# Kernel optimization log

Hardware: AMD Instinct MI355X
Metric: run time of the kernel (lower is better)

## Reference

```python
import jax, jax.numpy as jnp
import numpy as np

N, D, IN, HID, OUT, E = 20000, 8, 64, 128, 64, 100000
EPS = 1e-5


def _bn(h, g, b):
    # training-mode BatchNorm1d: biased batch variance, eps=1e-5
    m = h.mean(axis=0)
    v = jnp.mean((h - m) ** 2, axis=0)
    return (h - m) * jax.lax.rsqrt(v + EPS) * g + b


def setup_inputs() -> dict:
    key = jax.random.key(0)
    ks = jax.random.split(key, 12)
    x = jax.random.normal(ks[0], (N, IN), dtype=jnp.float32)
    node_ts = jax.random.uniform(ks[1], (N,), dtype=jnp.float32)
    neighbor_idx = jax.random.randint(ks[2], (N, D), 0, N, dtype=jnp.int32)
    neighbor_ts = jax.random.uniform(ks[3], (N, D), dtype=jnp.float32)
    target = jax.random.randint(ks[4], (2, E), 0, N, dtype=jnp.int32)
    neg_pairs = jax.random.randint(ks[5], (2, E), 0, N, dtype=jnp.int32)
    W1 = jax.random.normal(ks[6], (IN, HID), dtype=jnp.float32) * (1.0 / np.sqrt(IN))
    b1 = jnp.zeros((HID,), jnp.float32)
    g1 = jnp.ones((HID,), jnp.float32)
    be1 = jnp.zeros((HID,), jnp.float32)
    W2 = jax.random.normal(ks[7], (HID, OUT), dtype=jnp.float32) * (1.0 / np.sqrt(HID))
    b2 = jnp.zeros((OUT,), jnp.float32)
    g2 = jnp.ones((OUT,), jnp.float32)
    be2 = jnp.zeros((OUT,), jnp.float32)
    Wd = jax.random.normal(ks[8], (OUT, 1), dtype=jnp.float32) * (1.0 / np.sqrt(OUT))
    bd = jnp.zeros((1,), jnp.float32)
    return {"x": x, "node_ts": node_ts, "neighbor_idx": neighbor_idx,
            "neighbor_ts": neighbor_ts, "target": target, "neg_pairs": neg_pairs,
            "W1": W1, "b1": b1, "g1": g1, "be1": be1,
            "W2": W2, "b2": b2, "g2": g2, "be2": be2, "Wd": Wd, "bd": bd}


def reference(x, node_ts, neighbor_idx, neighbor_ts, target, neg_pairs,
              W1, b1, g1, be1, W2, b2, g2, be2, Wd, bd):
    n = jnp.arange(N, dtype=neighbor_idx.dtype)
    # ---- level-2 queries: every node at its own timestamp ----
    # children = D temporal-neighbor slots + self (self always valid, ts=node_ts)
    c_idx = jnp.concatenate([neighbor_idx, n[:, None]], axis=1)          # [N, D+1]
    c_ts = jnp.concatenate([neighbor_ts, node_ts[:, None]], axis=1)      # [N, D+1]
    mask2 = jnp.concatenate([neighbor_ts <= node_ts[:, None],
                             jnp.ones((N, 1), bool)], axis=1)            # [N, D+1]
    # ---- level-1 queries: each (child node, child ts) pair ----
    ci = c_idx.reshape(-1)                                               # [M]
    cts = c_ts.reshape(-1)
    gc_idx = jnp.concatenate([neighbor_idx[ci], ci[:, None]], axis=1)    # [M, D+1]
    mask1 = jnp.concatenate([neighbor_ts[ci] <= cts[:, None],
                             jnp.ones((ci.shape[0], 1), bool)], axis=1)
    # ---- layer 0: raw features of grandchildren ----
    h0 = x[gc_idx]                                                       # [M, D+1, IN]
    m1 = mask1.astype(x.dtype)
    agg1 = jnp.einsum('mk,mkf->mf', m1, h0) / m1.sum(1, keepdims=True)   # masked mean
    h1 = jax.nn.relu(_bn(agg1 @ W1 + b1, g1, be1))                       # [M, HID]
    h1 = h1.reshape(N, D + 1, HID)
    # ---- layer 2 aggregation over temporal children ----
    m2 = mask2.astype(x.dtype)
    agg2 = jnp.einsum('nk,nkf->nf', m2, h1) / m2.sum(1, keepdims=True)
    embs = jax.nn.relu(_bn(agg2 @ W2 + b2, g2, be2))                     # [N, OUT]
    # ---- HadNet link decoder + BCEWithLogits ----
    pos = (embs[target[0]] * embs[target[1]]) @ Wd + bd                  # [E, 1]
    neg = (embs[neg_pairs[0]] * embs[neg_pairs[1]]) @ Wd + bd            # [E, 1]
    preds = jnp.concatenate([pos, neg], axis=0)[:, 0]                    # [2E]
    labels = jnp.concatenate([jnp.ones((E,), x.dtype), jnp.zeros((E,), x.dtype)])
    loss = jnp.mean(jnp.maximum(preds, 0.0) - preds * labels
                    + jnp.log1p(jnp.exp(-jnp.abs(preds))))
    return loss
```

## Files before the change

### kernel.cpp

```cpp
#include <hip/hip_runtime.h>
#include <math.h>

constexpr int kN = 20000;
constexpr int kD = 8;
constexpr int kE = 100000;
constexpr int kM = kN * 9;
constexpr int kTiles1 = kM / 16;
constexpr int kTiles3 = kN / 16;
constexpr float kEps = 1e-5f;

constexpr int S_SUM1 = 0, S_SQ1 = 128, S_SUM2 = 256, S_SQ2 = 320;

constexpr size_t REG_B     = 23040000;
constexpr size_t OFF_AGG2  = 46080000;
constexpr size_t OFF_STATS = 51200000;
constexpr size_t OFF_PRE2  = 0;
constexpr size_t OFF_EMBS  = 5120000;
constexpr size_t OFF_EMBSW = 10240000;

typedef short short8 __attribute__((ext_vector_type(8)));
typedef float floatx4 __attribute__((ext_vector_type(4)));

__device__ __forceinline__ unsigned f2bf(float f) {
  unsigned u = __float_as_uint(f);
  u += 0x7fffu + ((u >> 16) & 1u);
  return u >> 16;
}

__global__ __launch_bounds__(256) void k1a_gather(
    const float* __restrict__ x, const float* __restrict__ node_ts,
    const int* __restrict__ nidx, const float* __restrict__ nts,
    unsigned short* __restrict__ agg1)
{
  const int m = blockIdx.x * 4 + (threadIdx.x >> 6);
  const int lane = threadIdx.x & 63;
  const int n = (int)((unsigned)m / 9u);
  const int slot = m - n * 9;
  int c; float t;
  if (slot < kD) { c = nidx[n * kD + slot]; t = nts[n * kD + slot]; }
  else           { c = n;                   t = node_ts[n]; }
  c = __builtin_amdgcn_readfirstlane(c);
  float s = x[c * 64 + lane];
  float fcnt = 1.f;
#pragma unroll
  for (int j = 0; j < kD; ++j) {
    int cj = nidx[c * kD + j];
    float w = (nts[c * kD + j] <= t) ? 1.f : 0.f;
    s = fmaf(w, x[cj * 64 + lane], s);
    fcnt += w;
  }
  float v = s / fcnt;
  const int tt = m >> 4, r = m & 15, g = lane >> 3, jj = lane & 7;
  agg1[tt * 1024 + g * 128 + r * 8 + jj] = (unsigned short)f2bf(v);
}

__global__ __launch_bounds__(256, 3) void k1b_gemm1(
    const unsigned short* aggA,
    unsigned short* preLo,
    unsigned short* __restrict__ preHi,
    const float* __restrict__ W1, const float* __restrict__ b1,
    float* __restrict__ stats)
{
  __shared__ unsigned short W1T[128 * 72];
  __shared__ float redS[256][8];
  __shared__ float redQ[256][8];

  const int tid = threadIdx.x;
  const int lane = tid & 63;
  const int wave = tid >> 6;
  const int l15 = lane & 15;
  const int q = lane >> 4;

  for (int i = tid; i < 8192; i += 256) {
    int n = i >> 6, k = i & 63;
    W1T[n * 72 + k] = (unsigned short)f2bf(W1[k * 128 + n]);
  }
  __syncthreads();

  short8 bf[8][2];
#pragma unroll
  for (int c = 0; c < 8; ++c)
#pragma unroll
    for (int s = 0; s < 2; ++s)
      bf[c][s] = *(const short8*)&W1T[(c * 16 + l15) * 72 + q * 8 + s * 32];

  float b1c[8];
#pragma unroll
  for (int c = 0; c < 8; ++c) b1c[c] = b1[c * 16 + l15];

  float sum8[8], sq8[8];
#pragma unroll
  for (int c = 0; c < 8; ++c) { sum8[c] = 0.f; sq8[c] = 0.f; }

  const int gw = blockIdx.x * 4 + wave;
  const int nw = gridDim.x * 4;

  for (int t = gw; t < kTiles1; t += nw) {
    const unsigned short* ap = aggA + (size_t)t * 1024;
    short8 af0 = *(const short8*)(ap + (q)*128 + l15 * 8);
    short8 af1 = *(const short8*)(ap + (4 + q) * 128 + l15 * 8);

    floatx4 acc[8];
#pragma unroll
    for (int c = 0; c < 8; ++c) {
      acc[c] = (floatx4){0.f, 0.f, 0.f, 0.f};
      acc[c] = __builtin_amdgcn_mfma_f32_16x16x32_bf16(af0, bf[c][0], acc[c], 0, 0, 0);
      acc[c] = __builtin_amdgcn_mfma_f32_16x16x32_bf16(af1, bf[c][1], acc[c], 0, 0, 0);
    }
#pragma unroll
    for (int c = 0; c < 8; ++c) {
      int colq = (c & 3) * 16 + l15;
#pragma unroll
      for (int i = 0; i < 4; ++i) {
        float v = acc[c][i] + b1c[c];
        int row = t * 16 + q * 4 + i;
        unsigned short hv = (unsigned short)f2bf(v);
        if (c < 4) preLo[(size_t)row * 64 + colq] = hv;
        else       preHi[(size_t)row * 64 + colq] = hv;
        sum8[c] += v; sq8[c] += v * v;
      }
    }
  }

  __syncthreads();
#pragma unroll
  for (int c = 0; c < 8; ++c) { redS[tid][c] = sum8[c]; redQ[tid][c] = sq8[c]; }
  __syncthreads();
  if (tid < 128) {
    int c = tid >> 4, r15 = tid & 15;
    float s = 0.f, qq = 0.f;
#pragma unroll
    for (int w = 0; w < 4; ++w)
#pragma unroll
      for (int p = 0; p < 4; ++p) {
        int T = w * 64 + p * 16 + r15;
        s += redS[T][c]; qq += redQ[T][c];
      }
    atomicAdd(&stats[S_SUM1 + tid], s);
    atomicAdd(&stats[S_SQ1 + tid], qq);
  }
}

__global__ __launch_bounds__(256) void k3a_agg2(
    const unsigned* __restrict__ loDW, const unsigned* __restrict__ hiDW,
    const float* __restrict__ node_ts, const float* __restrict__ nts,
    const float* __restrict__ stats, const float* __restrict__ g1,
    const float* __restrict__ be1, unsigned* __restrict__ agg2dw)
{
  __shared__ float sc[128], sh[128];
  const int tid = threadIdx.x;
  if (tid < 128) {
    float mean = stats[S_SUM1 + tid] * (1.f / kM);
    float var  = stats[S_SQ1 + tid] * (1.f / kM) - mean * mean;
    float s    = g1[tid] * rsqrtf(var + kEps);
    sc[tid] = s; sh[tid] = be1[tid] - mean * s;
  }
  __syncthreads();
  const int n = blockIdx.x * 4 + (tid >> 6);
  const int L = tid & 63;
  const unsigned* base = (L < 32) ? loDW : hiDW;
  const int Lc = L & 31;
  const float sc0 = sc[2 * L], sc1 = sc[2 * L + 1];
  const float sh0 = sh[2 * L], sh1 = sh[2 * L + 1];
  const float tn = node_ts[n];
  float s0 = 0.f, s1 = 0.f, fcnt = 0.f;
#pragma unroll
  for (int slot = 0; slot < 9; ++slot) {
    float w = (slot < kD) ? ((nts[n * kD + slot] <= tn) ? 1.f : 0.f) : 1.f;
    unsigned u = base[(size_t)(n * 9 + slot) * 32 + Lc];
    float p0 = __uint_as_float(u << 16);
    float p1 = __uint_as_float(u & 0xffff0000u);
    s0 += w * fmaxf(fmaf(p0, sc0, sh0), 0.f);
    s1 += w * fmaxf(fmaf(p1, sc1, sh1), 0.f);
    fcnt += w;
  }
  float r = 1.f / fcnt;
  agg2dw[n * 64 + L] = f2bf(s0 * r) | (f2bf(s1 * r) << 16);
}

__global__ __launch_bounds__(256, 3) void k3b_gemm2(
    const unsigned short* __restrict__ agg2, const float* __restrict__ W2,
    const float* __restrict__ b2, float* __restrict__ stats,
    float* __restrict__ pre2)
{
  __shared__ unsigned short W2T[64 * 136];
  __shared__ float redS[256][4];
  __shared__ float redQ[256][4];

  const int tid = threadIdx.x;
  const int lane = tid & 63;
  const int wave = tid >> 6;
  const int l15 = lane & 15;
  const int q = lane >> 4;

  for (int i = tid; i < 8192; i += 256) {
    int n = i >> 7, k = i & 127;
    W2T[n * 136 + k] = (unsigned short)f2bf(W2[k * 64 + n]);
  }
  __syncthreads();

  short8 bfr[4][4];
#pragma unroll
  for (int c = 0; c < 4; ++c)
#pragma unroll
    for (int s = 0; s < 4; ++s)
      bfr[c][s] = *(const short8*)&W2T[(c * 16 + l15) * 136 + q * 8 + s * 32];

  float b2c[4];
#pragma unroll
  for (int c = 0; c < 4; ++c) b2c[c] = b2[c * 16 + l15];

  float sum4[4], sq4[4];
#pragma unroll
  for (int c = 0; c < 4; ++c) { sum4[c] = 0.f; sq4[c] = 0.f; }

  const int gw = blockIdx.x * 4 + wave;
  const int nw = gridDim.x * 4;

  for (int t = gw; t < kTiles3; t += nw) {
    const int r0 = t * 16;
    short8 af[4];
#pragma unroll
    for (int s = 0; s < 4; ++s)
      af[s] = *(const short8*)&agg2[(size_t)(r0 + l15) * 128 + q * 8 + s * 32];

    floatx4 acc[4];
#pragma unroll
    for (int c = 0; c < 4; ++c) {
      acc[c] = (floatx4){0.f, 0.f, 0.f, 0.f};
#pragma unroll
      for (int s = 0; s < 4; ++s)
        acc[c] = __builtin_amdgcn_mfma_f32_16x16x32_bf16(af[s], bfr[c][s], acc[c], 0, 0, 0);
    }
#pragma unroll
    for (int c = 0; c < 4; ++c) {
      int col = c * 16 + l15;
#pragma unroll
      for (int i = 0; i < 4; ++i) {
        float v = acc[c][i] + b2c[c];
        int row = r0 + q * 4 + i;
        pre2[(size_t)row * 64 + col] = v;
        sum4[c] += v; sq4[c] += v * v;
      }
    }
  }

  __syncthreads();
#pragma unroll
  for (int c = 0; c < 4; ++c) { redS[tid][c] = sum4[c]; redQ[tid][c] = sq4[c]; }
  __syncthreads();
  if (tid < 64) {
    int c = tid >> 4, r15 = tid & 15;
    float s = 0.f, qq = 0.f;
#pragma unroll
    for (int w = 0; w < 4; ++w)
#pragma unroll
      for (int p = 0; p < 4; ++p) {
        int T = w * 64 + p * 16 + r15;
        s += redS[T][c]; qq += redQ[T][c];
      }
    atomicAdd(&stats[S_SUM2 + tid], s);
    atomicAdd(&stats[S_SQ2 + tid], qq);
  }
}

__global__ __launch_bounds__(256) void k5_embs(
    const float* __restrict__ pre2, const float* __restrict__ stats,
    const float* __restrict__ g2, const float* __restrict__ be2,
    const float* __restrict__ Wd, float* __restrict__ embs,
    float* __restrict__ embsW)
{
  __shared__ float sc[64], sh[64], wd[64];
  const int tid = threadIdx.x;
  if (tid < 64) {
    float mean = stats[S_SUM2 + tid] * (1.f / kN);
    float var  = stats[S_SQ2 + tid] * (1.f / kN) - mean * mean;
    float s    = g2[tid] * rsqrtf(var + kEps);
    sc[tid] = s; sh[tid] = be2[tid] - mean * s; wd[tid] = Wd[tid];
  }
  __syncthreads();
  int idx = blockIdx.x * 256 + tid;
  int col = idx & 63;
  float e = fmaxf(fmaf(pre2[idx], sc[col], sh[col]), 0.f);
  embs[idx] = e;
  embsW[idx] = e * wd[col];
}

__global__ __launch_bounds__(256) void k6_loss(
    const float* __restrict__ embs, const float* __restrict__ embsW,
    const int* __restrict__ tgt, const int* __restrict__ neg,
    const float* __restrict__ bd, float* __restrict__ out)
{
  __shared__ float redl[256];
  const int tid = threadIdx.x;
  const int tq = tid & 15;
  const int qb = tid >> 4;
  const float bd0 = bd[0];
  float lsum = 0.f;
  const int e0 = blockIdx.x * 128 + qb * 8;
#pragma unroll
  for (int it = 0; it < 8; ++it) {
    int e = e0 + it;
    if (e < 2 * kE) {
      int i, j; float lab;
      if (e < kE) { i = tgt[e];      j = tgt[kE + e]; lab = 1.f; }
      else        { i = neg[e - kE]; j = neg[e];      lab = 0.f; }
      float4 av = *(const float4*)(embsW + (size_t)i * 64 + tq * 4);
      float4 bv = *(const float4*)(embs  + (size_t)j * 64 + tq * 4);
      float p = av.x * bv.x + av.y * bv.y + av.z * bv.z + av.w * bv.w;
      p += __shfl_xor(p, 1); p += __shfl_xor(p, 2);
      p += __shfl_xor(p, 4); p += __shfl_xor(p, 8);
      p += bd0;
      float l = fmaxf(p, 0.f) - p * lab + log1pf(expf(-fabsf(p)));
      if (tq == 0) lsum += l;
    }
  }
  redl[tid] = lsum;
  __syncthreads();
  for (int s = 128; s > 0; s >>= 1) {
    if (tid < s) redl[tid] += redl[tid + s];
    __syncthreads();
  }
  if (tid == 0) atomicAdd(out, redl[0] * (1.f / (2 * kE)));
}

extern "C" void kernel_launch(void* const* d_in, const int* in_sizes, int n_in,
                              void* d_out, int out_size, void* d_ws, size_t ws_size,
                              hipStream_t stream) {
  (void)in_sizes; (void)n_in; (void)out_size; (void)ws_size;
  const float* x       = (const float*)d_in[0];
  const float* node_ts = (const float*)d_in[1];
  const int*   nidx    = (const int*)d_in[2];
  const float* nts     = (const float*)d_in[3];
  const int*   tgt     = (const int*)d_in[4];
  const int*   neg     = (const int*)d_in[5];
  const float* W1      = (const float*)d_in[6];
  const float* b1      = (const float*)d_in[7];
  const float* g1      = (const float*)d_in[8];
  const float* be1     = (const float*)d_in[9];
  const float* W2      = (const float*)d_in[10];
  const float* b2      = (const float*)d_in[11];
  const float* g2      = (const float*)d_in[12];
  const float* be2     = (const float*)d_in[13];
  const float* Wd      = (const float*)d_in[14];
  const float* bd      = (const float*)d_in[15];

  char* ws = (char*)d_ws;
  unsigned short* regA  = (unsigned short*)ws;
  unsigned short* regB  = (unsigned short*)(ws + REG_B);
  unsigned short* agg2  = (unsigned short*)(ws + OFF_AGG2);
  float* stats = (float*)(ws + OFF_STATS);
  float* pre2  = (float*)(ws + OFF_PRE2);
  float* embs  = (float*)(ws + OFF_EMBS);
  float* embsW = (float*)(ws + OFF_EMBSW);
  float* out   = (float*)d_out;

  hipMemsetAsync(stats, 0, 384 * sizeof(float), stream);
  hipMemsetAsync(out, 0, sizeof(float), stream);

  k1a_gather<<<kM / 4, 256, 0, stream>>>(x, node_ts, nidx, nts, regA);
  k1b_gemm1<<<704, 256, 0, stream>>>(regA, regA, regB, W1, b1, stats);
  k3a_agg2<<<kN / 4, 256, 0, stream>>>((const unsigned*)regA, (const unsigned*)regB,
                                       node_ts, nts, stats, g1, be1, (unsigned*)agg2);
  k3b_gemm2<<<160, 256, 0, stream>>>(agg2, W2, b2, stats, pre2);
  k5_embs<<<kN * 64 / 256, 256, 0, stream>>>(pre2, stats, g2, be2, Wd, embs, embsW);
  k6_loss<<<(2 * kE + 127) / 128, 256, 0, stream>>>(embs, embsW, tgt, neg, bd, out);
}
```

Measured before the change: 220.8 us.

## Recompute GEMM1 in fused apply kernel instead of storing pre-activations

The first GEMM now runs twice. One pass only accumulates BatchNorm statistics and no longer writes the bf16 pre-activation tensor. A new fused kernel recomputes the GEMM per 16-node group, applies BN and ReLU, and does the masked mean over temporal children through LDS atomics. This removes a large global write and read of the hidden activations in exchange for redundant MFMA work, W1 transposition in every block, and shared-memory atomics. The memset launches are also folded into existing kernels.

```diff
diff --git a/kernel.cpp b/kernel.cpp
--- a/kernel.cpp
+++ b/kernel.cpp
@@ -7,16 +7,16 @@
 constexpr int kM = kN * 9;
 constexpr int kTiles1 = kM / 16;
 constexpr int kTiles3 = kN / 16;
+constexpr int kGroups = kN / 16;
 constexpr float kEps = 1e-5f;
 
 constexpr int S_SUM1 = 0, S_SQ1 = 128, S_SUM2 = 256, S_SQ2 = 320;
 
-constexpr size_t REG_B     = 23040000;
-constexpr size_t OFF_AGG2  = 46080000;
-constexpr size_t OFF_STATS = 51200000;
-constexpr size_t OFF_PRE2  = 0;
-constexpr size_t OFF_EMBS  = 5120000;
-constexpr size_t OFF_EMBSW = 10240000;
+constexpr size_t OFF_AGG2  = 23040000;
+constexpr size_t OFF_PRE2  = 28160000;
+constexpr size_t OFF_EMBS  = 33280000;
+constexpr size_t OFF_EMBSW = 38400000;
+constexpr size_t OFF_STATS = 43520000;
 
 typedef short short8 __attribute__((ext_vector_type(8)));
 typedef float floatx4 __attribute__((ext_vector_type(4)));
@@ -30,8 +30,9 @@
 __global__ __launch_bounds__(256) void k1a_gather(
     const float* __restrict__ x, const float* __restrict__ node_ts,
     const int* __restrict__ nidx, const float* __restrict__ nts,
-    unsigned short* __restrict__ agg1)
-{
+    unsigned short* __restrict__ agg1, float* __restrict__ stats)
+{
+  if (blockIdx.x == 0 && threadIdx.x < 384) stats[threadIdx.x] = 0.f;
   const int m = blockIdx.x * 4 + (threadIdx.x >> 6);
   const int lane = threadIdx.x & 63;
   const int n = (int)((unsigned)m / 9u);
@@ -54,10 +55,8 @@
   agg1[tt * 1024 + g * 128 + r * 8 + jj] = (unsigned short)f2bf(v);
 }
 
-__global__ __launch_bounds__(256, 3) void k1b_gemm1(
-    const unsigned short* aggA,
-    unsigned short* preLo,
-    unsigned short* __restrict__ preHi,
+__global__ __launch_bounds__(256, 3) void k1s_stats(
+    const unsigned short* __restrict__ aggA,
     const float* __restrict__ W1, const float* __restrict__ b1,
     float* __restrict__ stats)
 {
@@ -97,7 +96,7 @@
 
   for (int t = gw; t < kTiles1; t += nw) {
     const unsigned short* ap = aggA + (size_t)t * 1024;
-    short8 af0 = *(const short8*)(ap + (q)*128 + l15 * 8);
+    short8 af0 = *(const short8*)(ap + q * 128 + l15 * 8);
     short8 af1 = *(const short8*)(ap + (4 + q) * 128 + l15 * 8);
 
     floatx4 acc[8];
@@ -108,18 +107,12 @@
       acc[c] = __builtin_amdgcn_mfma_f32_16x16x32_bf16(af1, bf[c][1], acc[c], 0, 0, 0);
     }
 #pragma unroll
-    for (int c = 0; c < 8; ++c) {
-      int colq = (c & 3) * 16 + l15;
+    for (int c = 0; c < 8; ++c)
 #pragma unroll
       for (int i = 0; i < 4; ++i) {
         float v = acc[c][i] + b1c[c];
-        int row = t * 16 + q * 4 + i;
-        unsigned short hv = (unsigned short)f2bf(v);
-        if (c < 4) preLo[(size_t)row * 64 + colq] = hv;
-        else       preHi[(size_t)row * 64 + colq] = hv;
         sum8[c] += v; sq8[c] += v * v;
       }
-    }
   }
 
   __syncthreads();
@@ -141,41 +134,104 @@
   }
 }
 
-__global__ __launch_bounds__(256) void k3a_agg2(
-    const unsigned* __restrict__ loDW, const unsigned* __restrict__ hiDW,
-    const float* __restrict__ node_ts, const float* __restrict__ nts,
-    const float* __restrict__ stats, const float* __restrict__ g1,
-    const float* __restrict__ be1, unsigned* __restrict__ agg2dw)
-{
+__global__ __launch_bounds__(256, 3) void k2_apply(
+    const unsigned short* __restrict__ aggA, const float* __restrict__ node_ts,
+    const float* __restrict__ nts, const float* __restrict__ W1,
+    const float* __restrict__ b1, const float* __restrict__ g1,
+    const float* __restrict__ be1, const float* __restrict__ stats,
+    unsigned* __restrict__ agg2dw)
+{
+  __shared__ unsigned short W1T[128 * 72];
   __shared__ float sc[128], sh[128];
+  __shared__ float wbuf[144];
+  __shared__ float rvs[16];
+  __shared__ float aggl[16 * 128];
+
   const int tid = threadIdx.x;
+  const int lane = tid & 63;
+  const int wave = tid >> 6;
+  const int l15 = lane & 15;
+  const int q = lane >> 4;
+  const int g = blockIdx.x;
+  const int n0 = g * 16;
+
+  for (int i = tid; i < 8192; i += 256) {
+    int n = i >> 6, k = i & 63;
+    W1T[n * 72 + k] = (unsigned short)f2bf(W1[k * 128 + n]);
+  }
   if (tid < 128) {
     float mean = stats[S_SUM1 + tid] * (1.f / kM);
     float var  = stats[S_SQ1 + tid] * (1.f / kM) - mean * mean;
     float s    = g1[tid] * rsqrtf(var + kEps);
     sc[tid] = s; sh[tid] = be1[tid] - mean * s;
   }
-  __syncthreads();
-  const int n = blockIdx.x * 4 + (tid >> 6);
-  const int L = tid & 63;
-  const unsigned* base = (L < 32) ? loDW : hiDW;
-  const int Lc = L & 31;
-  const float sc0 = sc[2 * L], sc1 = sc[2 * L + 1];
-  const float sh0 = sh[2 * L], sh1 = sh[2 * L + 1];
-  const float tn = node_ts[n];
-  float s0 = 0.f, s1 = 0.f, fcnt = 0.f;
-#pragma unroll
-  for (int slot = 0; slot < 9; ++slot) {
-    float w = (slot < kD) ? ((nts[n * kD + slot] <= tn) ? 1.f : 0.f) : 1.f;
-    unsigned u = base[(size_t)(n * 9 + slot) * 32 + Lc];
-    float p0 = __uint_as_float(u << 16);
-    float p1 = __uint_as_float(u & 0xffff0000u);
-    s0 += w * fmaxf(fmaf(p0, sc0, sh0), 0.f);
-    s1 += w * fmaxf(fmaf(p1, sc1, sh1), 0.f);
-    fcnt += w;
-  }
-  float r = 1.f / fcnt;
-  agg2dw[n * 64 + L] = f2bf(s0 * r) | (f2bf(s1 * r) << 16);
+  if (tid < 144) {
+    int nd = n0 + tid / 9, slot = tid % 9;
+    wbuf[tid] = (slot < kD) ? ((nts[nd * kD + slot] <= node_ts[nd]) ? 1.f : 0.f)
+                            : 1.f;
+  }
+  __syncthreads();
+
+  short8 bfr[8][2];
+#pragma unroll
+  for (int c = 0; c < 8; ++c)
+#pragma unroll
+    for (int s = 0; s < 2; ++s)
+      bfr[c][s] = *(const short8*)&W1T[(c * 16 + l15) * 72 + q * 8 + s * 32];
+
+  float scc[8], shc[8];
+#pragma unroll
+  for (int c = 0; c < 8; ++c) {
+    int col = c * 16 + l15;
+    scc[c] = sc[col];
+    shc[c] = fmaf(b1[col], sc[col], sh[col]);
+  }
+  if (tid < 16) {
+    float s = 0.f;
+#pragma unroll
+    for (int j = 0; j < 9; ++j) s += wbuf[tid * 9 + j];
+    rvs[tid] = 1.f / s;
+  }
+#pragma unroll
+  for (int p = 0; p < 8; ++p) aggl[tid + 256 * p] = 0.f;
+  __syncthreads();
+
+  for (int t9 = wave; t9 < 9; t9 += 4) {
+    const unsigned short* ap = aggA + (size_t)(g * 9 + t9) * 1024;
+    short8 af0 = *(const short8*)(ap + q * 128 + l15 * 8);
+    short8 af1 = *(const short8*)(ap + (4 + q) * 128 + l15 * 8);
+
+    floatx4 acc[8];
+#pragma unroll
+    for (int c = 0; c < 8; ++c) {
+      acc[c] = (floatx4){0.f, 0.f, 0.f, 0.f};
+      acc[c] = __builtin_amdgcn_mfma_f32_16x16x32_bf16(af0, bfr[c][0], acc[c], 0, 0, 0);
+      acc[c] = __builtin_amdgcn_mfma_f32_16x16x32_bf16(af1, bfr[c][1], acc[c], 0, 0, 0);
+    }
+#pragma unroll
+    for (int i = 0; i < 4; ++i) {
+      int r = t9 * 16 + q * 4 + i;
+      int ndl = (int)((unsigned)r / 9u);
+      float w = wbuf[r];
+#pragma unroll
+      for (int c = 0; c < 8; ++c) {
+        int col = c * 16 + l15;
+        float h = fmaxf(fmaf(acc[c][i], scc[c], shc[c]), 0.f);
+        atomicAdd(&aggl[ndl * 128 + col], w * h);
+      }
+    }
+  }
+  __syncthreads();
+
+#pragma unroll
+  for (int p = 0; p < 4; ++p) {
+    int idx = tid + 256 * p;
+    int ndl = idx >> 6, cp = idx & 63;
+    float r = rvs[ndl];
+    float v0 = aggl[ndl * 128 + 2 * cp] * r;
+    float v1 = aggl[ndl * 128 + 2 * cp + 1] * r;
+    agg2dw[(size_t)(n0 + ndl) * 64 + cp] = f2bf(v0) | (f2bf(v1) << 16);
+  }
 }
 
 __global__ __launch_bounds__(256, 3) void k3b_gemm2(
@@ -268,10 +324,11 @@
     const float* __restrict__ pre2, const float* __restrict__ stats,
     const float* __restrict__ g2, const float* __restrict__ be2,
     const float* __restrict__ Wd, float* __restrict__ embs,
-    float* __restrict__ embsW)
+    float* __restrict__ embsW, float* __restrict__ out)
 {
   __shared__ float sc[64], sh[64], wd[64];
   const int tid = threadIdx.x;
+  if (blockIdx.x == 0 && tid == 0) out[0] = 0.f;
   if (tid < 64) {
     float mean = stats[S_SUM2 + tid] * (1.f / kN);
     float var  = stats[S_SQ2 + tid] * (1.f / kN) - mean * mean;
@@ -346,23 +403,20 @@
   const float* bd      = (const float*)d_in[15];
 
   char* ws = (char*)d_ws;
-  unsigned short* regA  = (unsigned short*)ws;
-  unsigned short* regB  = (unsigned short*)(ws + REG_B);
-  unsigned short* agg2  = (unsigned short*)(ws + OFF_AGG2);
-  float* stats = (float*)(ws + OFF_STATS);
+  unsigned short* agg1 = (unsigned short*)ws;
+  unsigned short* agg2 = (unsigned short*)(ws + OFF_AGG2);
   float* pre2  = (float*)(ws + OFF_PRE2);
   float* embs  = (float*)(ws + OFF_EMBS);
   float* embsW = (float*)(ws + OFF_EMBSW);
+  float* stats = (float*)(ws + OFF_STATS);
   float* out   = (float*)d_out;
 
-  hipMemsetAsync(stats, 0, 384 * sizeof(float), stream);
-  hipMemsetAsync(out, 0, sizeof(float), stream);
-
-  k1a_gather<<<kM / 4, 256, 0, stream>>>(x, node_ts, nidx, nts, regA);
-  k1b_gemm1<<<704, 256, 0, stream>>>(regA, regA, regB, W1, b1, stats);
-  k3a_agg2<<<kN / 4, 256, 0, stream>>>((const unsigned*)regA, (const unsigned*)regB,
-                                       node_ts, nts, stats, g1, be1, (unsigned*)agg2);
+  k1a_gather<<<kM / 4, 256, 0, stream>>>(x, node_ts, nidx, nts, agg1, stats);
+  k1s_stats<<<512, 256, 0, stream>>>(agg1, W1, b1, stats);
+  k2_apply<<<kGroups, 256, 0, stream>>>(agg1, node_ts, nts, W1, b1, g1, be1,
+                                        stats, (unsigned*)agg2);
   k3b_gemm2<<<160, 256, 0, stream>>>(agg2, W2, b2, stats, pre2);
-  k5_embs<<<kN * 64 / 256, 256, 0, stream>>>(pre2, stats, g2, be2, Wd, embs, embsW);
+  k5_embs<<<kN * 64 / 256, 256, 0, stream>>>(pre2, stats, g2, be2, Wd, embs,
+                                             embsW, out);
   k6_loss<<<(2 * kE + 127) / 128, 256, 0, stream>>>(embs, embsW, tgt, neg, bd, out);
 }
```

After: 332.6 us. 50.6% more time.
